# Optimization experiments

Measured on AMD Instinct MI355X. Metric: run time of the kernel, lower is better.

The kernel has to match this reference:

```python
import jax, jax.numpy as jnp
import numpy as np

ROI = 268
K = 32
SLOPE = 0.33
EPS = 1e-5

def leaky(h):
    return jnp.where(h >= 0, h, SLOPE * h)

def bn(h, g, b):
    # BatchNorm in training mode: biased batch statistics over the node/batch axis
    mu = h.mean(0)
    var = ((h - mu) ** 2).mean(0)
    return (h - mu) * jax.lax.rsqrt(var + EPS) * g + b


def setup_inputs():
    B, F, C, deg = 64, ROI, 32, 32
    N = B * ROI
    key = jax.random.key(0)
    ks = jax.random.split(key, 32)
    x = jax.random.normal(ks[0], (N, F), jnp.float32)
    # static within-graph edges: every node has exactly `deg` incoming edges
    tgt = jnp.repeat(jnp.arange(N, dtype=jnp.int32), deg)
    src = (tgt // ROI) * ROI + jax.random.randint(ks[1], (N * deg,), 0, ROI, dtype=jnp.int32)
    edge_index = jnp.stack([src, tgt])
    batch = jnp.repeat(jnp.arange(B, dtype=jnp.int32), ROI)
    def lin(k, i, o):
        return 0.05 * jax.random.normal(k, (i, o), jnp.float32)
    def vec(k, o):
        return 0.05 * jax.random.normal(k, (o,), jnp.float32)
    p = dict(
        x=x, edge_index=edge_index, batch=batch,
        W1a=lin(ks[2], 2 * F, C), b1a=vec(ks[3], C), W1b=lin(ks[4], C, C), b1b=vec(ks[5], C),
        g1=1.0 + vec(ks[6], C), be1=vec(ks[7], C),
        W2a=lin(ks[8], 2 * F, C), b2a=vec(ks[9], C), W2b=lin(ks[10], C, C), b2b=vec(ks[11], C),
        g2=1.0 + vec(ks[12], C), be2=vec(ks[13], C),
        W3=lin(ks[14], 2 * F, 1), b3=vec(ks[15], 1), g3=1.0 + vec(ks[16], 1), be3=vec(ks[17], 1),
        Wl1=lin(ks[18], ROI + 2 * C, 256), bl1=vec(ks[19], 256), g4=1.0 + vec(ks[20], 256), be4=vec(ks[21], 256),
        Wl2=lin(ks[22], 256, 128), bl2=vec(ks[23], 128), g5=1.0 + vec(ks[24], 128), be5=vec(ks[25], 128),
        Wl3=lin(ks[26], 128, 1), bl3=vec(ks[27], 1),
    )
    return p


def reference(x, edge_index, batch,
              W1a, b1a, W1b, b1b, g1, be1,
              W2a, b2a, W2b, b2b, g2, be2,
              W3, b3, g3, be3,
              Wl1, bl1, g4, be4, Wl2, bl2, g5, be5, Wl3, bl3):
    N, F = x.shape
    B = N // ROI
    src, tgt = edge_index[0], edge_index[1]
    xi = x[tgt]                       # [E, F] central node feature
    xd = x[src] - xi                  # [E, F] x_j - x_i
    # --- gcn1: EdgeConv(mlp1) + BN + LeakyReLU (dropout = identity in eval) ---
    m1 = leaky(xi @ W1a[:F] + xd @ W1a[F:] + b1a) @ W1b + b1b   # [E, C]
    a1 = jax.ops.segment_max(m1, tgt, num_segments=N)
    a1 = jnp.where(jnp.isfinite(a1), a1, 0.0)
    x1 = leaky(bn(a1, g1, be1))
    # --- gcn3: EdgeConv(mlp3) + BN + LeakyReLU ---
    m3 = xi @ W3[:F] + xd @ W3[F:] + b3                          # [E, 1]
    a3 = jax.ops.segment_max(m3, tgt, num_segments=N)
    a3 = jnp.where(jnp.isfinite(a3), a3, 0.0)
    x3 = leaky(bn(a3, g3, be3))
    # --- gcn2: DynamicEdgeConv(mlp2, k=32) + BN + LeakyReLU ---
    xg = x.reshape(B, ROI, F)
    sq = jnp.sum(xg * xg, -1)
    d2 = sq[:, :, None] + sq[:, None, :] - 2.0 * jnp.einsum('bif,bjf->bij', xg, xg)
    _, idx = jax.lax.top_k(-d2, K)                               # [B, ROI, K], includes self
    xj = jax.vmap(lambda f, i: f[i])(xg, idx)                    # [B, ROI, K, F]
    part_i = jnp.einsum('bif,fc->bic', xg, W2a[:F])
    part_d = jnp.einsum('bikf,fc->bikc', xj - xg[:, :, None, :], W2a[F:])
    h2 = leaky(part_i[:, :, None, :] + part_d + b2a)
    m2 = h2 @ W2b + b2b                                          # [B, ROI, K, C]
    x2 = leaky(bn(m2.max(axis=2).reshape(N, -1), g2, be2))
    # --- readout ---
    counts = jax.ops.segment_sum(jnp.ones((N, 1), x.dtype), batch, num_segments=B)
    p1 = jax.ops.segment_sum(x1, batch, num_segments=B) / counts
    p2 = jax.ops.segment_sum(x2, batch, num_segments=B) / counts
    z = jnp.concatenate([p1, p2, x3.reshape(B, ROI)], -1)        # [B, 268+64]
    z = leaky(bn(z @ Wl1 + bl1, g4, be4))
    z = leaky(bn(z @ Wl2 + bl2, g5, be5))
    return z @ Wl3 + bl3                                          # [B, 1]
```

## Files before the change

### kernel.cpp

```cpp
#include <hip/hip_runtime.h>
#include <hip/hip_bf16.h>

#define ROI   268
#define FDIM  268
#define NB    64
#define NN    (NB*ROI)
#define CC    32
#define DEG   32
#define KSEL  32
#define SLOPE 0.33f
#define EPSBN 1e-5f

typedef __attribute__((ext_vector_type(8)))  short bf16x8;
typedef __attribute__((ext_vector_type(4)))  float f32x4;
typedef __attribute__((ext_vector_type(16))) float f32x16;

__device__ __forceinline__ float lrelu(float h) { return h >= 0.f ? h : SLOPE * h; }

__device__ __forceinline__ unsigned short f2bf(float f) {
    union { __hip_bfloat16 h; unsigned short s; } u;
    u.h = __float2bfloat16(f);
    return u.s;
}
__device__ __forceinline__ float bf2f(unsigned short h) {
    return __uint_as_float(((unsigned int)h) << 16);
}

#define PREP_PACK_BLOCKS  2448
#define PREP_PACKW_BLOCKS 18
#define PREP_SCAL_BLOCKS  1072

__global__ __launch_bounds__(256) void k_prep(
    const float* __restrict__ x,
    const float* __restrict__ W1a, const float* __restrict__ W2a,
    const float* __restrict__ W3,  const float* __restrict__ b3,
    unsigned short* __restrict__ Xh, unsigned short* __restrict__ Xl,
    unsigned short* __restrict__ Wfh, unsigned short* __restrict__ Wfl,
    float* __restrict__ u3, float* __restrict__ v3, float* __restrict__ sqv)
{
    const int bid = blockIdx.x;
    const int tid = threadIdx.x;
    if (bid < PREP_PACK_BLOCKS) {
        const int gid = bid * 256 + tid;
        const int l   = gid & 63;
        const int f3  = gid >> 6;
        const int ks  = f3 % 9;
        const int bc  = f3 / 9;
        const int ct  = bc % 17;
        const int b   = bc / 17;
        const int node = ct * 16 + (l & 15);
        const int k0   = ks * 32 + (l >> 4) * 8;
        float f[8];
        #pragma unroll
        for (int j = 0; j < 8; ++j) f[j] = 0.f;
        if (node < ROI) {
            const float* row = &x[((size_t)b * ROI + node) * FDIM];
            if (k0 + 3 < FDIM) { float4 v = *(const float4*)&row[k0];     f[0]=v.x; f[1]=v.y; f[2]=v.z; f[3]=v.w; }
            if (k0 + 7 < FDIM) { float4 v = *(const float4*)&row[k0 + 4]; f[4]=v.x; f[5]=v.y; f[6]=v.z; f[7]=v.w; }
        }
        unsigned short hh[8], ll[8];
        #pragma unroll
        for (int j = 0; j < 8; ++j) {
            hh[j] = f2bf(f[j]);
            ll[j] = f2bf(f[j] - bf2f(hh[j]));
        }
        uint4 hp, lp;
        hp.x = (unsigned)hh[0] | ((unsigned)hh[1] << 16); hp.y = (unsigned)hh[2] | ((unsigned)hh[3] << 16);
        hp.z = (unsigned)hh[4] | ((unsigned)hh[5] << 16); hp.w = (unsigned)hh[6] | ((unsigned)hh[7] << 16);
        lp.x = (unsigned)ll[0] | ((unsigned)ll[1] << 16); lp.y = (unsigned)ll[2] | ((unsigned)ll[3] << 16);
        lp.z = (unsigned)ll[4] | ((unsigned)ll[5] << 16); lp.w = (unsigned)ll[6] | ((unsigned)ll[7] << 16);
        const size_t base = (size_t)f3 * 512 + l * 8;
        *(uint4*)&Xh[base] = hp;
        *(uint4*)&Xl[base] = lp;
    } else if (bid < PREP_PACK_BLOCKS + PREP_PACKW_BLOCKS) {
        const int gid = (bid - PREP_PACK_BLOCKS) * 256 + tid;
        const int l  = gid & 63;
        const int f3 = gid >> 6;
        const int ks = f3 % 9;
        const int mc = f3 / 9;
        const int ct = mc & 1;
        const int m  = mc >> 1;
        const int k0 = ks * 32 + (l >> 4) * 8;
        const int c  = ct * 16 + (l & 15);
        const float* W = (m < 2) ? W1a : W2a;
        const bool isU = (m & 1) == 0;
        unsigned short hh[8], ll[8];
        #pragma unroll
        for (int j = 0; j < 8; ++j) {
            const int kk = k0 + j;
            float val = 0.f;
            if (kk < FDIM) {
                float wb = W[(size_t)(FDIM + kk) * CC + c];
                val = isU ? (W[(size_t)kk * CC + c] - wb) : wb;
            }
            hh[j] = f2bf(val);
            ll[j] = f2bf(val - bf2f(hh[j]));
        }
        uint4 hp, lp;
        hp.x = (unsigned)hh[0] | ((unsigned)hh[1] << 16); hp.y = (unsigned)hh[2] | ((unsigned)hh[3] << 16);
        hp.z = (unsigned)hh[4] | ((unsigned)hh[5] << 16); hp.w = (unsigned)hh[6] | ((unsigned)hh[7] << 16);
        lp.x = (unsigned)ll[0] | ((unsigned)ll[1] << 16); lp.y = (unsigned)ll[2] | ((unsigned)ll[3] << 16);
        lp.z = (unsigned)ll[4] | ((unsigned)ll[5] << 16); lp.w = (unsigned)ll[6] | ((unsigned)ll[7] << 16);
        const size_t base = (size_t)f3 * 512 + l * 8;
        *(uint4*)&Wfh[base] = hp;
        *(uint4*)&Wfl[base] = lp;
    } else {
        const int s = bid - (PREP_PACK_BLOCKS + PREP_PACKW_BLOCKS);
        const int l = tid & 63;
        #pragma unroll
        for (int i = 0; i < 4; ++i) {
            const int n = s * 16 + i * 4 + (tid >> 6);
            const float* row = &x[(size_t)n * FDIM];
            float su = 0.f, sv = 0.f, sq = 0.f;
            #pragma unroll
            for (int t = 0; t < 4; ++t) {
                const int f = l + 64 * t;
                float xv = row[f];
                float wv = W3[FDIM + f];
                float wu = W3[f] - wv;
                su += xv * wu; sv += xv * wv; sq += xv * xv;
            }
            if (l < 12) {
                const int f = 256 + l;
                float xv = row[f];
                float wv = W3[FDIM + f];
                float wu = W3[f] - wv;
                su += xv * wu; sv += xv * wv; sq += xv * xv;
            }
            #pragma unroll
            for (int mm = 32; mm > 0; mm >>= 1) {
                su += __shfl_xor(su, mm);
                sv += __shfl_xor(sv, mm);
                sq += __shfl_xor(sq, mm);
            }
            if (l == 0) {
                u3[n] = su + b3[0];
                v3[n] = sv;
                sqv[n] = sq;
            }
        }
    }
}

#define PD_DIST_BLOCKS 320
#define PD_PROJ_BLOCKS 1088

__global__ __launch_bounds__(256) void k_projdist(
    const unsigned short* __restrict__ Xh, const unsigned short* __restrict__ Xl,
    const unsigned short* __restrict__ Wfh, const unsigned short* __restrict__ Wfl,
    const float* __restrict__ b1a, const float* __restrict__ b2a,
    const float* __restrict__ sqv,
    float* __restrict__ u1, float* __restrict__ v1,
    float* __restrict__ u2, float* __restrict__ v2,
    float* __restrict__ d2)
{
    __shared__ __align__(16) unsigned short Bh_l[4608], Bl_l[4608];
    __shared__ float sqj[288];
    const int tid = threadIdx.x;
    const int l   = tid & 63;
    const int w   = tid >> 6;

    if (blockIdx.x >= PD_DIST_BLOCKS) {
        const int tile = blockIdx.x - PD_DIST_BLOCKS;
        const int b    = tile / 17;
        const int ctn  = tile % 17;
        bf16x8 Ah[9], Al[9];
        {
            const size_t abase = (size_t)tile * 9 * 512 + l * 8;
            #pragma unroll
            for (int ks = 0; ks < 9; ++ks) {
                Ah[ks] = *(const bf16x8*)&Xh[abase + ks * 512];
                Al[ks] = *(const bf16x8*)&Xl[abase + ks * 512];
            }
        }
        float* outp = (w == 0) ? u1 : (w == 1) ? v1 : (w == 2) ? u2 : v2;
        #pragma unroll
        for (int ct = 0; ct < 2; ++ct) {
            const size_t wbase = ((size_t)((w * 2 + ct) * 9)) * 512 + l * 8;
            f32x4 acc = {0.f, 0.f, 0.f, 0.f};
            #pragma unroll
            for (int ks = 0; ks < 9; ++ks) {
                bf16x8 bh = *(const bf16x8*)&Wfh[wbase + ks * 512];
                bf16x8 bl = *(const bf16x8*)&Wfl[wbase + ks * 512];
                acc = __builtin_amdgcn_mfma_f32_16x16x32_bf16(Ah[ks], bh, acc, 0, 0, 0);
                acc = __builtin_amdgcn_mfma_f32_16x16x32_bf16(Ah[ks], bl, acc, 0, 0, 0);
                acc = __builtin_amdgcn_mfma_f32_16x16x32_bf16(Al[ks], bh, acc, 0, 0, 0);
            }
            const int ch = ct * 16 + (l & 15);
            float bias = 0.f;
            if (w == 0) bias = b1a[ch];
            else if (w == 2) bias = b2a[ch];
            const int r0 = (l >> 4) * 4;
            #pragma unroll
            for (int i = 0; i < 4; ++i) {
                const int node = ctn * 16 + r0 + i;
                if (node < ROI)
                    outp[((size_t)b * ROI + node) * 32 + ch] = acc[i] + bias;
            }
        }
        return;
    }

    const int bid = blockIdx.x;
    const int b   = bid / 5;
    const int bx  = bid % 5;
    const int at  = min(bx * 4 + w, 16);
    const size_t bN = (size_t)b * ROI;

    for (int t = tid; t < 288; t += 256)
        sqj[t] = (t < ROI) ? sqv[bN + t] : __builtin_inff();

    bf16x8 Ah[9], Al[9];
    {
        const size_t abase = ((size_t)(b * 17 + at) * 9) * 512 + l * 8;
        #pragma unroll
        for (int ks = 0; ks < 9; ++ks) {
            Ah[ks] = *(const bf16x8*)&Xh[abase + ks * 512];
            Al[ks] = *(const bf16x8*)&Xl[abase + ks * 512];
        }
    }
    const int rbase = at * 16 + (l >> 4) * 4;
    float sqr4[4];
    #pragma unroll
    for (int i = 0; i < 4; ++i) {
        const int row = rbase + i;
        sqr4[i] = (row < ROI) ? sqv[bN + row] : 0.f;
    }

    float* drow = &d2[(size_t)b * 288 * 288];
    for (int ct = 0; ct < 17; ++ct) {
        __syncthreads();
        {
            const unsigned short* srcH = &Xh[((size_t)(b * 17 + ct) * 9) * 512];
            const unsigned short* srcL = &Xl[((size_t)(b * 17 + ct) * 9) * 512];
            for (int t = tid; t < 576; t += 256) {
                *(uint4*)&Bh_l[t * 8] = *(const uint4*)&srcH[t * 8];
                *(uint4*)&Bl_l[t * 8] = *(const uint4*)&srcL[t * 8];
            }
        }
        __syncthreads();
        f32x4 acc = {0.f, 0.f, 0.f, 0.f};
        #pragma unroll
        for (int ks = 0; ks < 9; ++ks) {
            bf16x8 bh = *(const bf16x8*)&Bh_l[ks * 512 + l * 8];
            bf16x8 bl = *(const bf16x8*)&Bl_l[ks * 512 + l * 8];
            acc = __builtin_amdgcn_mfma_f32_16x16x32_bf16(Ah[ks], bh, acc, 0, 0, 0);
            acc = __builtin_amdgcn_mfma_f32_16x16x32_bf16(Ah[ks], bl, acc, 0, 0, 0);
            acc = __builtin_amdgcn_mfma_f32_16x16x32_bf16(Al[ks], bh, acc, 0, 0, 0);
        }
        const int col = ct * 16 + (l & 15);
        const float sj = sqj[col];
        #pragma unroll
        for (int i = 0; i < 4; ++i)
            drow[(size_t)(rbase + i) * 288 + col] = sqr4[i] + sj - 2.f * acc[i];
    }
    for (int t = tid; t < 64 * 16; t += 256) {
        const int r = bx * 64 + (t >> 4);
        if (r < 288) drow[(size_t)r * 288 + 272 + (t & 15)] = __builtin_inff();
    }
}

__global__ __launch_bounds__(256) void k_sel(
    const float* __restrict__ d2, int* __restrict__ knn)
{
    const int grp = blockIdx.x * 8 + (threadIdx.x >> 5);
    const int sl  = threadIdx.x & 31;
    const int b   = grp / ROI;
    const int row = grp - b * ROI;
    const float* src = &d2[((size_t)b * 288 + row) * 288];

    unsigned k[9];
    #pragma unroll
    for (int q = 0; q < 9; ++q) {
        const int idx = q * 32 + sl;
        unsigned bits = __float_as_uint(src[idx]);
        unsigned msk  = (unsigned)(((int)bits) >> 31) | 0x80000000u;
        k[q] = ((bits ^ msk) & ~0x1FFu) | (unsigned)idx;
    }
    #pragma unroll
    for (int i = 1; i < 9; ++i) {
        #pragma unroll
        for (int j = i; j > 0; --j) {
            unsigned lo = k[j-1] < k[j] ? k[j-1] : k[j];
            unsigned hi = k[j-1] < k[j] ? k[j]   : k[j-1];
            k[j-1] = lo; k[j] = hi;
        }
    }
    unsigned keep = 0;
    #pragma unroll
    for (int it = 0; it < KSEL; ++it) {
        unsigned m = k[0];
        #pragma unroll
        for (int mm = 16; mm > 0; mm >>= 1) {
            unsigned o = (unsigned)__shfl_xor((int)m, mm, 32);
            m = o < m ? o : m;
        }
        if (sl == it) keep = m;
        const bool win = (k[0] == m);
        #pragma unroll
        for (int q = 0; q < 8; ++q) k[q] = win ? k[q+1] : k[q];
        k[8] = win ? 0xFFFFFFFFu : k[8];
    }
    knn[(size_t)grp * KSEL + sl] = b * ROI + (int)(keep & 0x1FFu);
}

__global__ __launch_bounds__(256) void k_edge_both(
    const float* __restrict__ u1, const float* __restrict__ v1,
    const float* __restrict__ W1b, const float* __restrict__ b1b,
    const int* __restrict__ ei,
    const float* __restrict__ u2, const float* __restrict__ v2,
    const float* __restrict__ W2b, const float* __restrict__ b2b,
    const int* __restrict__ knn,
    const float* __restrict__ u3, const float* __restrict__ v3,
    float* __restrict__ a1, float* __restrict__ a2, float* __restrict__ a3)
{
    const int tid  = threadIdx.x;
    const int l    = tid & 63;
    const int wv   = tid >> 6;
    const int half = l >> 5;
    const int e    = l & 31;
    const bool g1 = blockIdx.x < (NN / 16);
    const int  nb = g1 ? blockIdx.x : blockIdx.x - (NN / 16);
    const float* u  = g1 ? u1 : u2;
    const float* v  = g1 ? v1 : v2;
    const float* Wb = g1 ? W1b : W2b;
    const float* bb = g1 ? b1b : b2b;
    const int* nbr  = g1 ? ei : knn;
    float* aout     = g1 ? a1 : a2;

    union { bf16x8 v8; unsigned u4[4]; } B0, B1;
    #pragma unroll
    for (int j = 0; j < 4; ++j) {
        B0.u4[j] = (unsigned)f2bf(Wb[(half * 8 + 2*j    ) * 32 + e])
                 | ((unsigned)f2bf(Wb[(half * 8 + 2*j + 1) * 32 + e]) << 16);
        B1.u4[j] = (unsigned)f2bf(Wb[(16 + half * 8 + 2*j    ) * 32 + e])
                 | ((unsigned)f2bf(Wb[(16 + half * 8 + 2*j + 1) * 32 + e]) << 16);
    }
    const float biasc = bb[e];

    int jns[4];
    #pragma unroll
    for (int nn = 0; nn < 4; ++nn)
        jns[nn] = nbr[(size_t)(nb * 16 + wv * 4 + nn) * DEG + e];

    #pragma unroll 2
    for (int nn = 0; nn < 4; ++nn) {
        const int n  = nb * 16 + wv * 4 + nn;
        const int jn = jns[nn];

        float hv[16];
        #pragma unroll
        for (int s = 0; s < 2; ++s) {
            const int c0 = s * 16 + half * 8;
            float4 uv0 = *(const float4*)&u[(size_t)n  * 32 + c0];
            float4 uv1 = *(const float4*)&u[(size_t)n  * 32 + c0 + 4];
            float4 vv0 = *(const float4*)&v[(size_t)jn * 32 + c0];
            float4 vv1 = *(const float4*)&v[(size_t)jn * 32 + c0 + 4];
            hv[s*8+0] = lrelu(uv0.x + vv0.x);
            hv[s*8+1] = lrelu(uv0.y + vv0.y);
            hv[s*8+2] = lrelu(uv0.z + vv0.z);
            hv[s*8+3] = lrelu(uv0.w + vv0.w);
            hv[s*8+4] = lrelu(uv1.x + vv1.x);
            hv[s*8+5] = lrelu(uv1.y + vv1.y);
            hv[s*8+6] = lrelu(uv1.z + vv1.z);
            hv[s*8+7] = lrelu(uv1.w + vv1.w);
        }
        union { bf16x8 v8; unsigned u4[4]; } A0, A1;
        #pragma unroll
        for (int j = 0; j < 4; ++j) {
            A0.u4[j] = (unsigned)f2bf(hv[2*j])     | ((unsigned)f2bf(hv[2*j + 1]) << 16);
            A1.u4[j] = (unsigned)f2bf(hv[8 + 2*j]) | ((unsigned)f2bf(hv[8 + 2*j + 1]) << 16);
        }
        f32x16 acc = {0.f,0.f,0.f,0.f,0.f,0.f,0.f,0.f,0.f,0.f,0.f,0.f,0.f,0.f,0.f,0.f};
        acc = __builtin_amdgcn_mfma_f32_32x32x16_bf16(A0.v8, B0.v8, acc, 0, 0, 0);
        acc = __builtin_amdgcn_mfma_f32_32x32x16_bf16(A1.v8, B1.v8, acc, 0, 0, 0);

        float mx = acc[0];
        #pragma unroll
        for (int r = 1; r < 16; ++r) mx = fmaxf(mx, acc[r]);
        mx = fmaxf(mx, __shfl_xor(mx, 32));
        if (l < 32) aout[(size_t)n * 32 + l] = mx + biasc;

        if (g1) {
            float a3v = u3[n] + v3[jn];
            #pragma unroll
            for (int mm = 16; mm > 0; mm >>= 1) a3v = fmaxf(a3v, __shfl_xor(a3v, mm));
            if (l == 0) a3[n] = a3v;
        }
    }
}

__global__ __launch_bounds__(256) void k_stats1(
    const float* __restrict__ a1, const float* __restrict__ a2,
    float* __restrict__ part)
{
    const int p = blockIdx.x;
    const int tid = threadIdx.x;
    const int ch = tid & 31, sub = tid >> 5;
    const size_t base = (size_t)p * ROI;
    float s1 = 0.f, q1 = 0.f, s2 = 0.f, q2 = 0.f;
    for (int n = sub; n < ROI; n += 8) {
        float v1 = a1[(base + n) * 32 + ch];
        float v2 = a2[(base + n) * 32 + ch];
        s1 += v1; q1 += v1 * v1; s2 += v2; q2 += v2 * v2;
    }
    __shared__ float L[4][256];
    L[0][tid] = s1; L[1][tid] = q1; L[2][tid] = s2; L[3][tid] = q2;
    __syncthreads();
    if (tid < 128) {
        const int a = tid >> 5, c = tid & 31;
        float s = 0.f;
        #pragma unroll
        for (int k = 0; k < 8; ++k) s += L[a][c + 32 * k];
        part[p * 128 + a * 32 + c] = s;
    }
}

__global__ __launch_bounds__(256) void k_pool_fc1(
    const float* __restrict__ a1, const float* __restrict__ a2, const float* __restrict__ a3,
    const float* __restrict__ part,
    const float* __restrict__ g1, const float* __restrict__ be1,
    const float* __restrict__ g2, const float* __restrict__ be2,
    const float* __restrict__ g3, const float* __restrict__ be3,
    const float* __restrict__ Wl1, const float* __restrict__ bl1,
    float* __restrict__ h1)
{
    const int b = blockIdx.x, tid = threadIdx.x;
    __shared__ float stl[130];
    __shared__ float zs[332];
    __shared__ float P[4][64];
    __shared__ float S3[256], Q3[256];

    {
        float p0 = 0.f, p1 = 0.f, p2 = 0.f, p3 = 0.f;
        float q0 = 0.f, q1 = 0.f, q2 = 0.f, q3 = 0.f;
        int n = tid;
        for (; n + 768 < NN; n += 1024) {
            float a = a3[n], bb = a3[n + 256], c = a3[n + 512], d = a3[n + 768];
            p0 += a; q0 += a * a;
            p1 += bb; q1 += bb * bb;
            p2 += c; q2 += c * c;
            p3 += d; q3 += d * d;
        }
        for (; n < NN; n += 256) { float a = a3[n]; p0 += a; q0 += a * a; }
        S3[tid] = (p0 + p1) + (p2 + p3);
        Q3[tid] = (q0 + q1) + (q2 + q3);
    }
    __syncthreads();
    for (int off = 128; off > 0; off >>= 1) {
        if (tid < off) { S3[tid] += S3[tid + off]; Q3[tid] += Q3[tid + off]; }
        __syncthreads();
    }
    if (tid < 64) {
        const int a = (tid >> 5) * 2, c = tid & 31;
        float s0 = 0.f, s1 = 0.f, q0b = 0.f, q1b = 0.f;
        for (int p = 0; p < 64; p += 2) {
            s0  += part[p * 128 + a * 32 + c];
            q0b += part[p * 128 + (a + 1) * 32 + c];
            s1  += part[(p + 1) * 128 + a * 32 + c];
            q1b += part[(p + 1) * 128 + (a + 1) * 32 + c];
        }
        float ss = s0 + s1, qq = q0b + q1b;
        float gv = (tid < 32) ? g1[c] : g2[c];
        float bv = (tid < 32) ? be1[c] : be2[c];
        float mu  = ss * (1.f / NN);
        float var = qq * (1.f / NN) - mu * mu;
        float sc  = gv * rsqrtf(var + EPSBN);
        stl[tid * 2] = sc; stl[tid * 2 + 1] = bv - mu * sc;
    }
    if (tid == 64) {
        float mu  = S3[0] * (1.f / NN);
        float var = Q3[0] * (1.f / NN) - mu * mu;
        float sc  = g3[0] * rsqrtf(var + EPSBN);
        stl[128] = sc; stl[129] = be3[0] - mu * sc;
    }
    __syncthreads();

    const int c = tid & 63, grp = tid >> 6;
    const float* src = (c < 32) ? a1 : a2;
    const int ch = c & 31;
    const float sc = stl[c * 2], sh = stl[c * 2 + 1];
    {
        const size_t rb = (size_t)b * ROI;
        float p0 = 0.f, p1 = 0.f, p2 = 0.f, p3 = 0.f;
        int i = grp;
        for (; i + 12 < ROI; i += 16) {
            p0 += lrelu(src[(rb + i)      * 32 + ch] * sc + sh);
            p1 += lrelu(src[(rb + i + 4)  * 32 + ch] * sc + sh);
            p2 += lrelu(src[(rb + i + 8)  * 32 + ch] * sc + sh);
            p3 += lrelu(src[(rb + i + 12) * 32 + ch] * sc + sh);
        }
        for (; i < ROI; i += 4)
            p0 += lrelu(src[(rb + i) * 32 + ch] * sc + sh);
        P[grp][c] = (p0 + p1) + (p2 + p3);
    }
    const float sc3 = stl[128], sh3 = stl[129];
    for (int i = tid; i < ROI; i += 256)
        zs[64 + i] = lrelu(a3[b * ROI + i] * sc3 + sh3);
    __syncthreads();
    if (tid < 64)
        zs[tid] = (P[0][tid] + P[1][tid] + P[2][tid] + P[3][tid]) * (1.f / ROI);
    __syncthreads();

    {
        float s0 = 0.f, s1 = 0.f, s2 = 0.f, s3 = 0.f;
        #pragma unroll 4
        for (int k = 0; k < 332; k += 4) {
            s0 += zs[k]     * Wl1[(size_t)k       * 256 + tid];
            s1 += zs[k + 1] * Wl1[(size_t)(k + 1) * 256 + tid];
            s2 += zs[k + 2] * Wl1[(size_t)(k + 2) * 256 + tid];
            s3 += zs[k + 3] * Wl1[(size_t)(k + 3) * 256 + tid];
        }
        h1[(size_t)b * 256 + tid] = bl1[tid] + ((s0 + s1) + (s2 + s3));
    }
}

__global__ __launch_bounds__(128) void k_fc2s(
    const float* __restrict__ h1,
    const float* __restrict__ g4, const float* __restrict__ be4,
    const float* __restrict__ Wl2, const float* __restrict__ bl2,
    float* __restrict__ h2)
{
    const int b = blockIdx.x, tid = threadIdx.x;
    __shared__ float hs[256];
    float s0 = 0.f, q0 = 0.f, s1 = 0.f, q1 = 0.f;
    float s2 = 0.f, q2 = 0.f, s3 = 0.f, q3 = 0.f;
    for (int r = 0; r < NB; r += 2) {
        float a = h1[(size_t)r * 256 + tid];
        float c = h1[(size_t)r * 256 + tid + 128];
        float d = h1[(size_t)(r + 1) * 256 + tid];
        float e = h1[(size_t)(r + 1) * 256 + tid + 128];
        s0 += a; q0 += a * a;
        s1 += c; q1 += c * c;
        s2 += d; q2 += d * d;
        s3 += e; q3 += e * e;
    }
    {
        float ssA = s0 + s2, qqA = q0 + q2;
        float muA = ssA * (1.f / NB);
        float vaA = qqA * (1.f / NB) - muA * muA;
        float scA = g4[tid] * rsqrtf(vaA + EPSBN);
        float shA = be4[tid] - muA * scA;
        hs[tid] = lrelu(h1[(size_t)b * 256 + tid] * scA + shA);
        float ssB = s1 + s3, qqB = q1 + q3;
        float muB = ssB * (1.f / NB);
        float vaB = qqB * (1.f / NB) - muB * muB;
        float scB = g4[tid + 128] * rsqrtf(vaB + EPSBN);
        float shB = be4[tid + 128] - muB * scB;
        hs[tid + 128] = lrelu(h1[(size_t)b * 256 + tid + 128] * scB + shB);
    }
    __syncthreads();
    float s0b = 0.f, s1b = 0.f, s2b = 0.f, s3b = 0.f;
    #pragma unroll 4
    for (int k = 0; k < 256; k += 4) {
        s0b += hs[k]     * Wl2[(size_t)k       * 128 + tid];
        s1b += hs[k + 1] * Wl2[(size_t)(k + 1) * 128 + tid];
        s2b += hs[k + 2] * Wl2[(size_t)(k + 2) * 128 + tid];
        s3b += hs[k + 3] * Wl2[(size_t)(k + 3) * 128 + tid];
    }
    h2[(size_t)b * 128 + tid] = bl2[tid] + ((s0b + s1b) + (s2b + s3b));
}

__global__ __launch_bounds__(128) void k_fc3s(
    const float* __restrict__ h2,
    const float* __restrict__ g5, const float* __restrict__ be5,
    const float* __restrict__ Wl3, const float* __restrict__ bl3,
    float* __restrict__ out)
{
    const int tid = threadIdx.x;
    __shared__ float T[64][133];
    float s0 = 0.f, q0 = 0.f, s1 = 0.f, q1 = 0.f;
    for (int r = 0; r < NB; r += 2) {
        float a = h2[(size_t)r * 128 + tid];
        float b = h2[(size_t)(r + 1) * 128 + tid];
        s0 += a; q0 += a * a;
        s1 += b; q1 += b * b;
    }
    float ss = s0 + s1, qq = q0 + q1;
    float mu  = ss * (1.f / NB);
    float var = qq * (1.f / NB) - mu * mu;
    float sc  = g5[tid] * rsqrtf(var + EPSBN);
    float sh  = be5[tid] - mu * sc;
    const float w3 = Wl3[tid];
    for (int r = 0; r < NB; ++r)
        T[r][tid] = lrelu(h2[(size_t)r * 128 + tid] * sc + sh) * w3;
    __syncthreads();
    if (tid < 64) {
        float a0 = 0.f, a1 = 0.f, a2 = 0.f, a3 = 0.f;
        #pragma unroll 4
        for (int c = 0; c < 128; c += 4) {
            a0 += T[tid][c];
            a1 += T[tid][c + 1];
            a2 += T[tid][c + 2];
            a3 += T[tid][c + 3];
        }
        out[tid] = bl3[0] + ((a0 + a1) + (a2 + a3));
    }
}

extern "C" void kernel_launch(void* const* d_in, const int* in_sizes, int n_in,
                              void* d_out, int out_size, void* d_ws, size_t ws_size,
                              hipStream_t stream)
{
    (void)in_sizes; (void)n_in; (void)out_size; (void)ws_size;
    const float* x   = (const float*)d_in[0];
    const int*   ei  = (const int*)d_in[1];
    const float* W1a = (const float*)d_in[3];
    const float* b1a = (const float*)d_in[4];
    const float* W1b = (const float*)d_in[5];
    const float* b1b = (const float*)d_in[6];
    const float* g1  = (const float*)d_in[7];
    const float* be1 = (const float*)d_in[8];
    const float* W2a = (const float*)d_in[9];
    const float* b2a = (const float*)d_in[10];
    const float* W2b = (const float*)d_in[11];
    const float* b2b = (const float*)d_in[12];
    const float* g2  = (const float*)d_in[13];
    const float* be2 = (const float*)d_in[14];
    const float* W3  = (const float*)d_in[15];
    const float* b3  = (const float*)d_in[16];
    const float* g3  = (const float*)d_in[17];
    const float* be3 = (const float*)d_in[18];
    const float* Wl1 = (const float*)d_in[19];
    const float* bl1 = (const float*)d_in[20];
    const float* g4  = (const float*)d_in[21];
    const float* be4 = (const float*)d_in[22];
    const float* Wl2 = (const float*)d_in[23];
    const float* bl2 = (const float*)d_in[24];
    const float* g5  = (const float*)d_in[25];
    const float* be5 = (const float*)d_in[26];
    const float* Wl3 = (const float*)d_in[27];
    const float* bl3 = (const float*)d_in[28];

    float* ws  = (float*)d_ws;
    float* u1  = ws;
    float* v1  = u1 + (size_t)NN * 32;
    float* u2  = v1 + (size_t)NN * 32;
    float* v2  = u2 + (size_t)NN * 32;
    float* u3  = v2 + (size_t)NN * 32;
    float* v3  = u3 + NN;
    float* sqv = v3 + NN;
    float* a1  = sqv + NN;
    float* a2  = a1 + (size_t)NN * 32;
    float* a3  = a2 + (size_t)NN * 32;
    int*   knn = (int*)(a3 + NN);
    float* h1  = (float*)(knn + (size_t)NN * 32);
    float* h2  = h1 + (size_t)NB * 256;
    float* part = h2 + (size_t)NB * 128;
    unsigned short* Xh = (unsigned short*)(((uintptr_t)(part + 64 * 128) + 255) & ~(uintptr_t)255);
    unsigned short* Xl = Xh + (size_t)64 * 17 * 9 * 512;
    float* d2 = (float*)(((uintptr_t)(Xl + (size_t)64 * 17 * 9 * 512) + 255) & ~(uintptr_t)255);
    unsigned short* Wfh = (unsigned short*)(d2 + (size_t)64 * 288 * 288);
    unsigned short* Wfl = Wfh + (size_t)8 * 9 * 512;

    k_prep<<<PREP_PACK_BLOCKS + PREP_PACKW_BLOCKS + PREP_SCAL_BLOCKS, 256, 0, stream>>>(
        x, W1a, W2a, W3, b3, Xh, Xl, Wfh, Wfl, u3, v3, sqv);
    k_projdist<<<PD_DIST_BLOCKS + PD_PROJ_BLOCKS, 256, 0, stream>>>(
        Xh, Xl, Wfh, Wfl, b1a, b2a, sqv, u1, v1, u2, v2, d2);
    k_sel<<<NN / 8, 256, 0, stream>>>(d2, knn);
    k_edge_both<<<2 * (NN / 16), 256, 0, stream>>>(u1, v1, W1b, b1b, ei,
                                                   u2, v2, W2b, b2b, knn,
                                                   u3, v3, a1, a2, a3);
    k_stats1<<<64, 256, 0, stream>>>(a1, a2, part);
    k_pool_fc1<<<NB, 256, 0, stream>>>(a1, a2, a3, part, g1, be1, g2, be2, g3, be3,
                                       Wl1, bl1, h1);
    k_fc2s<<<NB, 128, 0, stream>>>(h1, g4, be4, Wl2, bl2, h2);
    k_fc3s<<<1, 128, 0, stream>>>(h2, g5, be5, Wl3, bl3, (float*)d_out);
}
```

Before: 147.5 us.

## Fuse top-k neighbor selection into edge kernel and widen projdist blocks

Result: no change. 148.4 us (+0.6%).

```diff
diff --git a/kernel.cpp b/kernel.cpp
--- a/kernel.cpp
+++ b/kernel.cpp
@@ -142,10 +142,10 @@
     }
 }
 
-#define PD_DIST_BLOCKS 320
+#define PD_DIST_BLOCKS 192
 #define PD_PROJ_BLOCKS 1088
 
-__global__ __launch_bounds__(256) void k_projdist(
+__global__ __launch_bounds__(512) void k_projdist(
     const unsigned short* __restrict__ Xh, const unsigned short* __restrict__ Xl,
     const unsigned short* __restrict__ Wfh, const unsigned short* __restrict__ Wfl,
     const float* __restrict__ b1a, const float* __restrict__ b2a,
@@ -164,6 +164,8 @@
         const int tile = blockIdx.x - PD_DIST_BLOCKS;
         const int b    = tile / 17;
         const int ctn  = tile % 17;
+        const int m    = w >> 1;
+        const int ct   = w & 1;
         bf16x8 Ah[9], Al[9];
         {
             const size_t abase = (size_t)tile * 9 * 512 + l * 8;
@@ -173,41 +175,38 @@
                 Al[ks] = *(const bf16x8*)&Xl[abase + ks * 512];
             }
         }
-        float* outp = (w == 0) ? u1 : (w == 1) ? v1 : (w == 2) ? u2 : v2;
-        #pragma unroll
-        for (int ct = 0; ct < 2; ++ct) {
-            const size_t wbase = ((size_t)((w * 2 + ct) * 9)) * 512 + l * 8;
-            f32x4 acc = {0.f, 0.f, 0.f, 0.f};
-            #pragma unroll
-            for (int ks = 0; ks < 9; ++ks) {
-                bf16x8 bh = *(const bf16x8*)&Wfh[wbase + ks * 512];
-                bf16x8 bl = *(const bf16x8*)&Wfl[wbase + ks * 512];
-                acc = __builtin_amdgcn_mfma_f32_16x16x32_bf16(Ah[ks], bh, acc, 0, 0, 0);
-                acc = __builtin_amdgcn_mfma_f32_16x16x32_bf16(Ah[ks], bl, acc, 0, 0, 0);
-                acc = __builtin_amdgcn_mfma_f32_16x16x32_bf16(Al[ks], bh, acc, 0, 0, 0);
-            }
-            const int ch = ct * 16 + (l & 15);
-            float bias = 0.f;
-            if (w == 0) bias = b1a[ch];
-            else if (w == 2) bias = b2a[ch];
-            const int r0 = (l >> 4) * 4;
-            #pragma unroll
-            for (int i = 0; i < 4; ++i) {
-                const int node = ctn * 16 + r0 + i;
-                if (node < ROI)
-                    outp[((size_t)b * ROI + node) * 32 + ch] = acc[i] + bias;
-            }
+        float* outp = (m == 0) ? u1 : (m == 1) ? v1 : (m == 2) ? u2 : v2;
+        const size_t wbase = ((size_t)((m * 2 + ct) * 9)) * 512 + l * 8;
+        f32x4 acc = {0.f, 0.f, 0.f, 0.f};
+        #pragma unroll
+        for (int ks = 0; ks < 9; ++ks) {
+            bf16x8 bh = *(const bf16x8*)&Wfh[wbase + ks * 512];
+            bf16x8 bl = *(const bf16x8*)&Wfl[wbase + ks * 512];
+            acc = __builtin_amdgcn_mfma_f32_16x16x32_bf16(Ah[ks], bh, acc, 0, 0, 0);
+            acc = __builtin_amdgcn_mfma_f32_16x16x32_bf16(Ah[ks], bl, acc, 0, 0, 0);
+            acc = __builtin_amdgcn_mfma_f32_16x16x32_bf16(Al[ks], bh, acc, 0, 0, 0);
+        }
+        const int ch = ct * 16 + (l & 15);
+        float bias = 0.f;
+        if (m == 0) bias = b1a[ch];
+        else if (m == 2) bias = b2a[ch];
+        const int r0 = (l >> 4) * 4;
+        #pragma unroll
+        for (int i = 0; i < 4; ++i) {
+            const int node = ctn * 16 + r0 + i;
+            if (node < ROI)
+                outp[((size_t)b * ROI + node) * 32 + ch] = acc[i] + bias;
         }
         return;
     }
 
     const int bid = blockIdx.x;
-    const int b   = bid / 5;
-    const int bx  = bid % 5;
-    const int at  = min(bx * 4 + w, 16);
+    const int b   = bid / 3;
+    const int bx  = bid % 3;
+    const int at  = min(bx * 8 + w, 16);
     const size_t bN = (size_t)b * ROI;
 
-    for (int t = tid; t < 288; t += 256)
+    for (int t = tid; t < 288; t += 512)
         sqj[t] = (t < ROI) ? sqv[bN + t] : __builtin_inff();
 
     bf16x8 Ah[9], Al[9];
@@ -233,7 +232,7 @@
         {
             const unsigned short* srcH = &Xh[((size_t)(b * 17 + ct) * 9) * 512];
             const unsigned short* srcL = &Xl[((size_t)(b * 17 + ct) * 9) * 512];
-            for (int t = tid; t < 576; t += 256) {
+            for (int t = tid; t < 576; t += 512) {
                 *(uint4*)&Bh_l[t * 8] = *(const uint4*)&srcH[t * 8];
                 *(uint4*)&Bl_l[t * 8] = *(const uint4*)&srcL[t * 8];
             }
@@ -254,54 +253,10 @@
         for (int i = 0; i < 4; ++i)
             drow[(size_t)(rbase + i) * 288 + col] = sqr4[i] + sj - 2.f * acc[i];
     }
-    for (int t = tid; t < 64 * 16; t += 256) {
-        const int r = bx * 64 + (t >> 4);
+    for (int t = tid; t < 128 * 16; t += 512) {
+        const int r = bx * 128 + (t >> 4);
         if (r < 288) drow[(size_t)r * 288 + 272 + (t & 15)] = __builtin_inff();
     }
-}
-
-__global__ __launch_bounds__(256) void k_sel(
-    const float* __restrict__ d2, int* __restrict__ knn)
-{
-    const int grp = blockIdx.x * 8 + (threadIdx.x >> 5);
-    const int sl  = threadIdx.x & 31;
-    const int b   = grp / ROI;
-    const int row = grp - b * ROI;
-    const float* src = &d2[((size_t)b * 288 + row) * 288];
-
-    unsigned k[9];
-    #pragma unroll
-    for (int q = 0; q < 9; ++q) {
-        const int idx = q * 32 + sl;
-        unsigned bits = __float_as_uint(src[idx]);
-        unsigned msk  = (unsigned)(((int)bits) >> 31) | 0x80000000u;
-        k[q] = ((bits ^ msk) & ~0x1FFu) | (unsigned)idx;
-    }
-    #pragma unroll
-    for (int i = 1; i < 9; ++i) {
-        #pragma unroll
-        for (int j = i; j > 0; --j) {
-            unsigned lo = k[j-1] < k[j] ? k[j-1] : k[j];
-            unsigned hi = k[j-1] < k[j] ? k[j]   : k[j-1];
-            k[j-1] = lo; k[j] = hi;
-        }
-    }
-    unsigned keep = 0;
-    #pragma unroll
-    for (int it = 0; it < KSEL; ++it) {
-        unsigned m = k[0];
-        #pragma unroll
-        for (int mm = 16; mm > 0; mm >>= 1) {
-            unsigned o = (unsigned)__shfl_xor((int)m, mm, 32);
-            m = o < m ? o : m;
-        }
-        if (sl == it) keep = m;
-        const bool win = (k[0] == m);
-        #pragma unroll
-        for (int q = 0; q < 8; ++q) k[q] = win ? k[q+1] : k[q];
-        k[8] = win ? 0xFFFFFFFFu : k[8];
-    }
-    knn[(size_t)grp * KSEL + sl] = b * ROI + (int)(keep & 0x1FFu);
 }
 
 __global__ __launch_bounds__(256) void k_edge_both(
@@ -310,10 +265,11 @@
     const int* __restrict__ ei,
     const float* __restrict__ u2, const float* __restrict__ v2,
     const float* __restrict__ W2b, const float* __restrict__ b2b,
-    const int* __restrict__ knn,
+    const float* __restrict__ d2,
     const float* __restrict__ u3, const float* __restrict__ v3,
     float* __restrict__ a1, float* __restrict__ a2, float* __restrict__ a3)
 {
+    __shared__ int jn_l[16][32];
     const int tid  = threadIdx.x;
     const int l    = tid & 63;
     const int wv   = tid >> 6;
@@ -325,7 +281,6 @@
     const float* v  = g1 ? v1 : v2;
     const float* Wb = g1 ? W1b : W2b;
     const float* bb = g1 ? b1b : b2b;
-    const int* nbr  = g1 ? ei : knn;
     float* aout     = g1 ? a1 : a2;
 
     union { bf16x8 v8; unsigned u4[4]; } B0, B1;
@@ -339,9 +294,57 @@
     const float biasc = bb[e];
 
     int jns[4];
-    #pragma unroll
-    for (int nn = 0; nn < 4; ++nn)
-        jns[nn] = nbr[(size_t)(nb * 16 + wv * 4 + nn) * DEG + e];
+    if (g1) {
+        #pragma unroll
+        for (int nn = 0; nn < 4; ++nn)
+            jns[nn] = ei[(size_t)(nb * 16 + wv * 4 + nn) * DEG + e];
+    } else {
+        const int grp8 = tid >> 5;
+        const int sl   = tid & 31;
+        for (int r = 0; r < 2; ++r) {
+            const int n   = nb * 16 + grp8 * 2 + r;
+            const int b   = n / ROI;
+            const int row = n - b * ROI;
+            const float* src = &d2[((size_t)b * 288 + row) * 288];
+            unsigned k[9];
+            #pragma unroll
+            for (int q = 0; q < 9; ++q) {
+                const int idx = q * 32 + sl;
+                unsigned bits = __float_as_uint(src[idx]);
+                unsigned msk  = (unsigned)(((int)bits) >> 31) | 0x80000000u;
+                k[q] = ((bits ^ msk) & ~0x1FFu) | (unsigned)idx;
+            }
+            #pragma unroll
+            for (int i = 1; i < 9; ++i) {
+                #pragma unroll
+                for (int j = i; j > 0; --j) {
+                    unsigned lo = k[j-1] < k[j] ? k[j-1] : k[j];
+                    unsigned hi = k[j-1] < k[j] ? k[j]   : k[j-1];
+                    k[j-1] = lo; k[j] = hi;
+                }
+            }
+            unsigned keep = 0;
+            #pragma unroll
+            for (int it = 0; it < KSEL; ++it) {
+                unsigned m = k[0];
+                #pragma unroll
+                for (int mm = 16; mm > 0; mm >>= 1) {
+                    unsigned o = (unsigned)__shfl_xor((int)m, mm, 32);
+                    m = o < m ? o : m;
+                }
+                if (sl == it) keep = m;
+                const bool win = (k[0] == m);
+                #pragma unroll
+                for (int q = 0; q < 8; ++q) k[q] = win ? k[q+1] : k[q];
+                k[8] = win ? 0xFFFFFFFFu : k[8];
+            }
+            jn_l[grp8 * 2 + r][sl] = b * ROI + (int)(keep & 0x1FFu);
+        }
+        __syncthreads();
+        #pragma unroll
+        for (int nn = 0; nn < 4; ++nn)
+            jns[nn] = jn_l[wv * 4 + nn][e];
+    }
 
     #pragma unroll 2
     for (int nn = 0; nn < 4; ++nn) {
@@ -643,8 +646,7 @@
     float* a1  = sqv + NN;
     float* a2  = a1 + (size_t)NN * 32;
     float* a3  = a2 + (size_t)NN * 32;
-    int*   knn = (int*)(a3 + NN);
-    float* h1  = (float*)(knn + (size_t)NN * 32);
+    float* h1  = a3 + NN;
     float* h2  = h1 + (size_t)NB * 256;
     float* part = h2 + (size_t)NB * 128;
     unsigned short* Xh = (unsigned short*)(((uintptr_t)(part + 64 * 128) + 255) & ~(uintptr_t)255);
@@ -655,11 +657,10 @@
 
     k_prep<<<PREP_PACK_BLOCKS + PREP_PACKW_BLOCKS + PREP_SCAL_BLOCKS, 256, 0, stream>>>(
         x, W1a, W2a, W3, b3, Xh, Xl, Wfh, Wfl, u3, v3, sqv);
-    k_projdist<<<PD_DIST_BLOCKS + PD_PROJ_BLOCKS, 256, 0, stream>>>(
+    k_projdist<<<PD_DIST_BLOCKS + PD_PROJ_BLOCKS, 512, 0, stream>>>(
         Xh, Xl, Wfh, Wfl, b1a, b2a, sqv, u1, v1, u2, v2, d2);
-    k_sel<<<NN / 8, 256, 0, stream>>>(d2, knn);
     k_edge_both<<<2 * (NN / 16), 256, 0, stream>>>(u1, v1, W1b, b1b, ei,
-                                                   u2, v2, W2b, b2b, knn,
+                                                   u2, v2, W2b, b2b, d2,
                                                    u3, v3, a1, a2, a3);
     k_stats1<<<64, 256, 0, stream>>>(a1, a2, part);
     k_pool_fc1<<<NB, 256, 0, stream>>>(a1, a2, a3, part, g1, be1, g2, be2, g3, be3,
```
